# Kernel optimization log

Measured on AMD Instinct MI355X. Metric: run time of the kernel, lower is better.

## Reference

```python
import jax, jax.numpy as jnp
import numpy as np

N = 50000   # num_nodes
E = 640000  # num_edges (avg degree ~12.8)
D = 128     # input_dim
H = 128     # hidden_dim
T = 100     # targets per head


def setup_inputs() -> dict:
    key = jax.random.key(0)
    ks = jax.random.split(key, 20)
    w = lambda k, s: jax.random.normal(k, s, jnp.float32) * 0.02
    return {
        "x": jax.random.normal(ks[0], (N, D), jnp.float32),
        "edge_index": jax.random.randint(ks[1], (2, E), 0, N, dtype=jnp.int32),
        "edge_weight": jax.random.uniform(ks[2], (E,), jnp.float32),
        "ace_idx": jax.random.randint(ks[3], (T,), 0, N, dtype=jnp.int32),
        "h2_idx": jax.random.randint(ks[4], (T,), 0, N, dtype=jnp.int32),
        "W1": w(ks[5], (D, H)), "b1": jnp.zeros((H,), jnp.float32),
        "W2": w(ks[6], (H, H)), "b2": jnp.zeros((H,), jnp.float32),
        "W3": w(ks[7], (H, H)), "b3": jnp.zeros((H,), jnp.float32),
        "Wh": w(ks[8], (H, H)), "bh": jnp.zeros((H,), jnp.float32),
        "Wace": w(ks[9], (H, 1)), "bace": jnp.zeros((1,), jnp.float32),
        "Wh2": w(ks[10], (H, 1)), "bh2": jnp.zeros((1,), jnp.float32),
    }


def gcn_conv(x, src, dst, ew, W, b):
    # PyG GCNConv: add self-loops (weight 1), symmetric D^-1/2 (A+I) D^-1/2, then XW + b
    n = x.shape[0]
    xw = x @ W                                             # [N, H]
    deg = jax.ops.segment_sum(ew, dst, num_segments=n) + 1.0  # +1 from self-loop
    dinv = jax.lax.rsqrt(jnp.maximum(deg, 1e-12))          # deg >= 1 here
    norm = dinv[src] * ew * dinv[dst]                      # per-edge coefficient
    agg = jax.ops.segment_sum(norm[:, None] * xw[src], dst, num_segments=n)
    agg = agg + (dinv * dinv)[:, None] * xw                # self-loop contribution
    return agg + b


def reference(x, edge_index, edge_weight, ace_idx, h2_idx,
              W1, b1, W2, b2, W3, b3, Wh, bh, Wace, bace, Wh2, bh2):
    src, dst = edge_index[0], edge_index[1]
    h = jax.nn.relu(gcn_conv(x, src, dst, edge_weight, W1, b1))
    h = jax.nn.relu(gcn_conv(h, src, dst, edge_weight, W2, b2))
    h = jax.nn.relu(gcn_conv(h, src, dst, edge_weight, W3, b3))
    # dropout is identity in eval mode
    h = jax.nn.relu(h @ Wh + bh)
    ace_pred = h[ace_idx] @ Wace + bace   # [T, 1]
    h2_pred = h[h2_idx] @ Wh2 + bh2       # [T, 1]
    return jnp.concatenate([ace_pred, h2_pred], axis=0)  # [2T, 1]
```

## Files before the change

kernel.cpp:

```cpp
#include <hip/hip_runtime.h>
#include <math.h>

constexpr int N = 50000;
constexpr int E = 640000;
constexpr int D = 128;
constexpr int T = 100;
constexpr int NB = (N + 255) / 256;
constexpr int MAXDEG = 64;
constexpr float SC = 256.0f;
constexpr float SCINV = 1.0f / 256.0f;

typedef __attribute__((ext_vector_type(8))) _Float16 half8v;
typedef __attribute__((ext_vector_type(8))) unsigned short ushort8v;
typedef __attribute__((ext_vector_type(4))) float f32x4;


__global__ void edge_pass_kernel(const float* __restrict__ ew, const int* __restrict__ src,
                                 const int* __restrict__ dst,
                                 unsigned long long* __restrict__ degcnt,
                                 unsigned int* __restrict__ slot) {
  int e = blockIdx.x * 256 + threadIdx.x;
  if (e < E) {
    float w = ew[e];
    int d = dst[e];
    unsigned int fxdeg = __float2uint_rn(w * 16777216.0f);
    unsigned int fx16 = __float2uint_rn(w * 65536.0f);
    if (fx16 > 65535u) fx16 = 65535u;
    unsigned long long old = atomicAdd(&degcnt[d],
                                       ((unsigned long long)fxdeg << 32) | 1ull);
    unsigned int rank = (unsigned int)(old & 0xffffffffull);
    if (rank < MAXDEG)
      slot[(size_t)d * MAXDEG + rank] = (fx16 << 16) | (unsigned int)src[e];
  }
}


__global__ __launch_bounds__(256) void prep_kernel(
    const uint2* __restrict__ degcnt, float* __restrict__ dinv,
    const float* __restrict__ W0, const float* __restrict__ W1,
    const float* __restrict__ W2, unsigned short* __restrict__ wt,
    unsigned short* __restrict__ w3kn) {
  if (blockIdx.x < NB) {
    int i = blockIdx.x * 256 + threadIdx.x;
    if (i < N) {
      uint2 p = degcnt[i];
      float d = (float)p.y * (1.0f / 16777216.0f) + 1.0f;
      dinv[i] = 1.0f / sqrtf(d);
    }
  } else {
    int idx = (blockIdx.x - NB) * 256 + threadIdx.x;
    int layer = idx >> 14;
    int r = idx & 16383;
    int k = r & 127, n = r >> 7;
    const float* W = layer == 0 ? W0 : layer == 1 ? W1 : W2;
    float v = W[k * D + n] * (layer == 0 ? SC : 1.0f);
    _Float16 h = (_Float16)v;
    unsigned short bits = *(unsigned short*)&h;
    wt[layer * 16384 + n * D + k] = bits;
    if (layer == 2) w3kn[k * D + n] = bits;
  }
}


__device__ inline void stage_B(const unsigned short* __restrict__ Wt,
                               unsigned short* __restrict__ Bl, int tid) {
  constexpr int SB = 136;
#pragma unroll
  for (int it = 0; it < 8; ++it) {
    int idx = tid + it * 256;
    int r = idx >> 4;
    int c8 = idx & 15;
    ushort8v v = *(const ushort8v*)&Wt[r * D + c8 * 8];
    *(ushort8v*)&Bl[r * SB + c8 * 8] = v;
  }
}

__device__ inline void mfma_core_and_store(
    const unsigned short* __restrict__ Bl, half8v (*a)[2], const float* __restrict__ dinv,
    int row0, int rbase, int q, int n16, unsigned short* __restrict__ out) {
  constexpr int SB = 136;
  f32x4 acc[2][8] = {};
#pragma unroll
  for (int kc = 0; kc < 4; ++kc) {
    const int ko = kc * 32 + q * 8;
#pragma unroll
    for (int ct = 0; ct < 8; ++ct) {
      int n = ct * 16 + n16;
      half8v b = *(const half8v*)&Bl[n * SB + ko];
#pragma unroll
      for (int rt = 0; rt < 2; ++rt) {
        acc[rt][ct] = __builtin_amdgcn_mfma_f32_16x16x32_f16(a[kc][rt], b, acc[rt][ct], 0, 0, 0);
      }
    }
  }
#pragma unroll
  for (int rt = 0; rt < 2; ++rt) {
#pragma unroll
    for (int r = 0; r < 4; ++r) {
      int gr = row0 + rbase + rt * 16 + q * 4 + r;
      if (gr < N) {
        float dv = dinv[gr];
#pragma unroll
        for (int ct = 0; ct < 8; ++ct) {
          int col = ct * 16 + n16;
          _Float16 h = (_Float16)(acc[rt][ct][r] * dv);
          out[(size_t)gr * D + col] = *(unsigned short*)&h;
        }
      }
    }
  }
}

__global__ __launch_bounds__(256) void gemm_mfma_kernel(
    const unsigned short* __restrict__ A, const unsigned short* __restrict__ Wt,
    const float* __restrict__ dinv, unsigned short* __restrict__ out) {
  constexpr int SB = 136;
  __shared__ unsigned short Bl[128 * SB];
  const int tid = threadIdx.x;
  const int row0 = blockIdx.x * 128;
  stage_B(Wt, Bl, tid);
  __syncthreads();

  const int w = tid >> 6, lane = tid & 63;
  const int q = lane >> 4, n16 = lane & 15;
  const int rbase = w * 32;
  size_t arow[2];
#pragma unroll
  for (int rt = 0; rt < 2; ++rt) {
    int gr = row0 + rbase + rt * 16 + n16;
    if (gr >= N) gr = N - 1;
    arow[rt] = (size_t)gr * D;
  }
  half8v a[4][2];
#pragma unroll
  for (int kc = 0; kc < 4; ++kc) {
    const int ko = kc * 32 + q * 8;
#pragma unroll
    for (int rt = 0; rt < 2; ++rt)
      a[kc][rt] = *(const half8v*)&A[arow[rt] + ko];
  }
  mfma_core_and_store(Bl, a, dinv, row0, rbase, q, n16, out);
}

__global__ __launch_bounds__(256) void gemm_mfma_f32_kernel(
    const float* __restrict__ A, const unsigned short* __restrict__ Wt,
    const float* __restrict__ dinv, unsigned short* __restrict__ out) {
  constexpr int SB = 136;
  __shared__ unsigned short Bl[128 * SB];
  const int tid = threadIdx.x;
  const int row0 = blockIdx.x * 128;
  stage_B(Wt, Bl, tid);
  __syncthreads();

  const int w = tid >> 6, lane = tid & 63;
  const int q = lane >> 4, n16 = lane & 15;
  const int rbase = w * 32;
  size_t arow[2];
#pragma unroll
  for (int rt = 0; rt < 2; ++rt) {
    int gr = row0 + rbase + rt * 16 + n16;
    if (gr >= N) gr = N - 1;
    arow[rt] = (size_t)gr * D;
  }
  half8v a[4][2];
#pragma unroll
  for (int kc = 0; kc < 4; ++kc) {
    const int ko = kc * 32 + q * 8;
#pragma unroll
    for (int rt = 0; rt < 2; ++rt) {
      float4 v0 = *(const float4*)&A[arow[rt] + ko];
      float4 v1 = *(const float4*)&A[arow[rt] + ko + 4];
      half8v h;
      h[0] = (_Float16)v0.x; h[1] = (_Float16)v0.y;
      h[2] = (_Float16)v0.z; h[3] = (_Float16)v0.w;
      h[4] = (_Float16)v1.x; h[5] = (_Float16)v1.y;
      h[6] = (_Float16)v1.z; h[7] = (_Float16)v1.w;
      a[kc][rt] = h;
    }
  }
  mfma_core_and_store(Bl, a, dinv, row0, rbase, q, n16, out);
}


__global__ __launch_bounds__(256) void agg_kernel(
    const unsigned short* __restrict__ z, const unsigned int* __restrict__ slot,
    const uint2* __restrict__ degcnt, const float* __restrict__ dinv,
    const float* __restrict__ bias, unsigned short* __restrict__ oP) {
  int g = (blockIdx.x * 256 + threadIdx.x) >> 4;
  int lane = threadIdx.x & 15;

  int cnt = (int)degcnt[g].x; if (cnt > MAXDEG) cnt = MAXDEG;
  half8v xv = *(const half8v*)&z[(size_t)g * D + lane * 8];
  float acc[8];
#pragma unroll
  for (int i = 0; i < 8; ++i) acc[i] = (float)xv[i];

  const unsigned int* sl = slot + (size_t)g * MAXDEG;
  int k = 0;
  for (; k + 2 <= cnt; k += 2) {
    unsigned int p0 = sl[k], p1 = sl[k + 1];
    float c0 = (float)(p0 >> 16) * (1.0f / 65536.0f);
    float c1 = (float)(p1 >> 16) * (1.0f / 65536.0f);
    half8v v0 = *(const half8v*)&z[(size_t)(p0 & 0xffffu) * D + lane * 8];
    half8v v1 = *(const half8v*)&z[(size_t)(p1 & 0xffffu) * D + lane * 8];
#pragma unroll
    for (int i = 0; i < 8; ++i) {
      acc[i] = fmaf(c0, (float)v0[i], acc[i]);
      acc[i] = fmaf(c1, (float)v1[i], acc[i]);
    }
  }
  if (k < cnt) {
    unsigned int p = sl[k];
    float c = (float)(p >> 16) * (1.0f / 65536.0f);
    half8v v = *(const half8v*)&z[(size_t)(p & 0xffffu) * D + lane * 8];
#pragma unroll
    for (int i = 0; i < 8; ++i) acc[i] = fmaf(c, (float)v[i], acc[i]);
  }

  float dv = dinv[g];
  half8v hv;
#pragma unroll
  for (int i = 0; i < 8; ++i)
    hv[i] = (_Float16)fmaxf(fmaf(dv, acc[i], bias[lane * 8 + i] * SC), 0.f);
  *(half8v*)&oP[(size_t)g * D + lane * 8] = hv;
}


__global__ __launch_bounds__(256) void l23_heads_kernel(
    const unsigned short* __restrict__ z2, const unsigned int* __restrict__ slot,
    const uint2* __restrict__ degcnt, const float* __restrict__ dinv,
    const float* __restrict__ b2, const float* __restrict__ b3,
    const unsigned short* __restrict__ w3kn,
    const float* __restrict__ Wh, const float* __restrict__ bh,
    const int* __restrict__ ace_idx, const int* __restrict__ h2_idx,
    const float* __restrict__ Wace, const float* __restrict__ bace,
    const float* __restrict__ Wh2, const float* __restrict__ bh2,
    float* __restrict__ out) {
  __shared__ float sacc[16][128];
  __shared__ unsigned short w3l[16384];
  __shared__ float svec[128];
  __shared__ float h3v[128];
  __shared__ float psum[2];
  int t = blockIdx.x;
  int tid = threadIdx.x;
  int node; const float* whead; float bhead;
  if (t < T) { node = ace_idx[t];     whead = Wace; bhead = bace[0]; }
  else       { node = h2_idx[t - T];  whead = Wh2;  bhead = bh2[0]; }

#pragma unroll
  for (int it = 0; it < 8; ++it) {
    int idx = tid + it * 256;
    *(ushort8v*)&w3l[idx * 8] = *(const ushort8v*)&w3kn[idx * 8];
  }

  int grp = tid >> 4, lane = tid & 15;
  float b2l[8];
#pragma unroll
  for (int i = 0; i < 8; ++i) b2l[i] = b2[lane * 8 + i] * SC;

  int tcnt = (int)degcnt[node].x; if (tcnt > MAXDEG) tcnt = MAXDEG;
  const unsigned int* tsl = slot + (size_t)node * MAXDEG;
  int nitems = 1 + tcnt;
  float a[8] = {};
  for (int it = grp; it < nitems; it += 16) {
    int u; float wgt;
    if (it == 0) { u = node; wgt = 1.0f; }
    else {
      unsigned int p = tsl[it - 1];
      wgt = (float)(p >> 16) * (1.0f / 65536.0f);
      u = (int)(p & 0xffffu);
    }
    float dvu = dinv[u];
    half8v xv = *(const half8v*)&z2[(size_t)u * D + lane * 8];
    float r[8];
#pragma unroll
    for (int i = 0; i < 8; ++i) r[i] = (float)xv[i];
    int cu = (int)degcnt[u].x; if (cu > MAXDEG) cu = MAXDEG;
    const unsigned int* usl = slot + (size_t)u * MAXDEG;
    for (int e = 0; e < cu; ++e) {
      unsigned int p2 = usl[e];
      float c2 = (float)(p2 >> 16) * (1.0f / 65536.0f);
      half8v v = *(const half8v*)&z2[(size_t)(p2 & 0xffffu) * D + lane * 8];
#pragma unroll
      for (int i = 0; i < 8; ++i) r[i] = fmaf(c2, (float)v[i], r[i]);
    }
#pragma unroll
    for (int i = 0; i < 8; ++i) {
      float h2 = fmaxf(fmaf(dvu, r[i], b2l[i]), 0.f);
      a[i] = fmaf(wgt, dvu * h2, a[i]);
    }
  }
#pragma unroll
  for (int i = 0; i < 8; ++i) sacc[grp][lane * 8 + i] = a[i];
  __syncthreads();

  if (tid < 128) {
    float s = 0.f;
#pragma unroll
    for (int gp = 0; gp < 16; ++gp) s += sacc[gp][tid];
    svec[tid] = s * dinv[node];
  }
  __syncthreads();

  if (tid < 128) {
    float y = b3[tid] * SC;
#pragma unroll 16
    for (int k = 0; k < 128; ++k) {
      _Float16 wv = *(const _Float16*)&w3l[k * D + tid];
      y = fmaf(svec[k], (float)wv, y);
    }
    h3v[tid] = fmaxf(y, 0.f) * SCINV;
  }
  __syncthreads();

  float v = 0.f;
  if (tid < 128) {
    float acc = bh[tid];
#pragma unroll 16
    for (int k = 0; k < 128; ++k)
      acc = fmaf(h3v[k], Wh[k * D + tid], acc);
    v = fmaxf(acc, 0.f) * whead[tid];
  }
#pragma unroll
  for (int off = 32; off; off >>= 1) v += __shfl_down(v, off, 64);
  if (tid < 128 && (tid & 63) == 0) psum[tid >> 6] = v;
  __syncthreads();
  if (tid == 0) out[t] = psum[0] + psum[1] + bhead;
}


extern "C" void kernel_launch(void* const* d_in, const int* in_sizes, int n_in,
                              void* d_out, int out_size, void* d_ws, size_t ws_size,
                              hipStream_t stream) {
  const float* x    = (const float*)d_in[0];
  const int*   ei   = (const int*)d_in[1];
  const float* ew   = (const float*)d_in[2];
  const int*   ace  = (const int*)d_in[3];
  const int*   h2   = (const int*)d_in[4];
  const float* W1 = (const float*)d_in[5];  const float* b1 = (const float*)d_in[6];
  const float* W2 = (const float*)d_in[7];  const float* b2 = (const float*)d_in[8];
  const float* W3 = (const float*)d_in[9];  const float* b3 = (const float*)d_in[10];
  const float* Wh = (const float*)d_in[11]; const float* bh = (const float*)d_in[12];
  const float* Wace = (const float*)d_in[13]; const float* bace = (const float*)d_in[14];
  const float* Wh2  = (const float*)d_in[15]; const float* bh2  = (const float*)d_in[16];
  const int* src = ei;
  const int* dst = ei + E;

  char* w = (char*)d_ws;
  unsigned long long* degcnt = (unsigned long long*)w;  w += (size_t)N * 8;
  float* dinv   = (float*)w;              w += N * 4;
  unsigned int* slot = (unsigned int*)w;  w += (size_t)N * MAXDEG * 4;
  unsigned short* wt = (unsigned short*)w; w += 3 * 16384 * 2;
  unsigned short* w3kn = (unsigned short*)w; w += 16384 * 2;
  unsigned short* zbuf = (unsigned short*)w; w += (size_t)N * D * 2;
  unsigned short* P1  = (unsigned short*)w; w += (size_t)N * D * 2;

  hipMemsetAsync(degcnt, 0, (size_t)N * 8, stream);
  edge_pass_kernel<<<(E + 255) / 256, 256, 0, stream>>>(ew, src, dst, degcnt, slot);
  prep_kernel<<<NB + 192, 256, 0, stream>>>((const uint2*)degcnt, dinv, W1, W2, W3, wt, w3kn);

  const int GB = (N + 127) / 128;
  const int AG = N * 16 / 256;

  gemm_mfma_f32_kernel<<<GB, 256, 0, stream>>>(x, wt + 0 * 16384, dinv, zbuf);
  agg_kernel<<<AG, 256, 0, stream>>>(zbuf, slot, (const uint2*)degcnt, dinv, b1, P1);
  gemm_mfma_kernel<<<GB, 256, 0, stream>>>(P1, wt + 1 * 16384, dinv, zbuf);
  l23_heads_kernel<<<2 * T, 256, 0, stream>>>(zbuf, slot, (const uint2*)degcnt, dinv,
                                              b2, b3, w3kn, Wh, bh, ace, h2,
                                              Wace, bace, Wh2, bh2, (float*)d_out);
}
```

Measured before the change: 224.0 us.

## Fuse layer-1 aggregation into layer-2 GEMM via LDS tile

Merges the aggregation kernel and the second MFMA GEMM into one kernel. Each block aggregates 128 rows into an LDS tile, then runs the GEMM from LDS. This drops the intermediate P1 write and read through global memory, plus one launch. In exchange each block uses about 70KB of LDS, which lowers occupancy. The gather phase also runs in 8 serial passes per block, with fewer gather threads in flight than the standalone aggregation kernel had.

```diff
diff --git a/kernel.cpp b/kernel.cpp
--- a/kernel.cpp
+++ b/kernel.cpp
@@ -111,36 +111,6 @@
   }
 }
 
-__global__ __launch_bounds__(256) void gemm_mfma_kernel(
-    const unsigned short* __restrict__ A, const unsigned short* __restrict__ Wt,
-    const float* __restrict__ dinv, unsigned short* __restrict__ out) {
-  constexpr int SB = 136;
-  __shared__ unsigned short Bl[128 * SB];
-  const int tid = threadIdx.x;
-  const int row0 = blockIdx.x * 128;
-  stage_B(Wt, Bl, tid);
-  __syncthreads();
-
-  const int w = tid >> 6, lane = tid & 63;
-  const int q = lane >> 4, n16 = lane & 15;
-  const int rbase = w * 32;
-  size_t arow[2];
-#pragma unroll
-  for (int rt = 0; rt < 2; ++rt) {
-    int gr = row0 + rbase + rt * 16 + n16;
-    if (gr >= N) gr = N - 1;
-    arow[rt] = (size_t)gr * D;
-  }
-  half8v a[4][2];
-#pragma unroll
-  for (int kc = 0; kc < 4; ++kc) {
-    const int ko = kc * 32 + q * 8;
-#pragma unroll
-    for (int rt = 0; rt < 2; ++rt)
-      a[kc][rt] = *(const half8v*)&A[arow[rt] + ko];
-  }
-  mfma_core_and_store(Bl, a, dinv, row0, rbase, q, n16, out);
-}
 
 __global__ __launch_bounds__(256) void gemm_mfma_f32_kernel(
     const float* __restrict__ A, const unsigned short* __restrict__ Wt,
@@ -182,47 +152,76 @@
 }
 
 
-__global__ __launch_bounds__(256) void agg_kernel(
-    const unsigned short* __restrict__ z, const unsigned int* __restrict__ slot,
+__global__ __launch_bounds__(256) void agg_gemm_kernel(
+    const unsigned short* __restrict__ z1, const unsigned int* __restrict__ slot,
     const uint2* __restrict__ degcnt, const float* __restrict__ dinv,
-    const float* __restrict__ bias, unsigned short* __restrict__ oP) {
-  int g = (blockIdx.x * 256 + threadIdx.x) >> 4;
-  int lane = threadIdx.x & 15;
-
-  int cnt = (int)degcnt[g].x; if (cnt > MAXDEG) cnt = MAXDEG;
-  half8v xv = *(const half8v*)&z[(size_t)g * D + lane * 8];
-  float acc[8];
-#pragma unroll
-  for (int i = 0; i < 8; ++i) acc[i] = (float)xv[i];
-
-  const unsigned int* sl = slot + (size_t)g * MAXDEG;
-  int k = 0;
-  for (; k + 2 <= cnt; k += 2) {
-    unsigned int p0 = sl[k], p1 = sl[k + 1];
-    float c0 = (float)(p0 >> 16) * (1.0f / 65536.0f);
-    float c1 = (float)(p1 >> 16) * (1.0f / 65536.0f);
-    half8v v0 = *(const half8v*)&z[(size_t)(p0 & 0xffffu) * D + lane * 8];
-    half8v v1 = *(const half8v*)&z[(size_t)(p1 & 0xffffu) * D + lane * 8];
+    const float* __restrict__ bias, const unsigned short* __restrict__ Wt,
+    unsigned short* __restrict__ out) {
+  constexpr int SB = 136;
+  __shared__ unsigned short Bl[128 * SB];
+  __shared__ unsigned short Xl[128 * SB];
+  const int tid = threadIdx.x;
+  const int row0 = blockIdx.x * 128;
+  stage_B(Wt, Bl, tid);
+
+  const int grp = tid >> 4, lane = tid & 15;
+  float bl[8];
+#pragma unroll
+  for (int i = 0; i < 8; ++i) bl[i] = bias[lane * 8 + i] * SC;
+
+#pragma unroll
+  for (int pass = 0; pass < 8; ++pass) {
+    int r = pass * 16 + grp;
+    int g = row0 + r; if (g >= N) g = N - 1;
+    int cnt = (int)degcnt[g].x; if (cnt > MAXDEG) cnt = MAXDEG;
+    half8v xv = *(const half8v*)&z1[(size_t)g * D + lane * 8];
+    float acc[8];
+#pragma unroll
+    for (int i = 0; i < 8; ++i) acc[i] = (float)xv[i];
+    const unsigned int* sl = slot + (size_t)g * MAXDEG;
+    int k = 0;
+    for (; k + 2 <= cnt; k += 2) {
+      unsigned int p0 = sl[k], p1 = sl[k + 1];
+      float c0 = (float)(p0 >> 16) * (1.0f / 65536.0f);
+      float c1 = (float)(p1 >> 16) * (1.0f / 65536.0f);
+      half8v v0 = *(const half8v*)&z1[(size_t)(p0 & 0xffffu) * D + lane * 8];
+      half8v v1 = *(const half8v*)&z1[(size_t)(p1 & 0xffffu) * D + lane * 8];
+#pragma unroll
+      for (int i = 0; i < 8; ++i) {
+        acc[i] = fmaf(c0, (float)v0[i], acc[i]);
+        acc[i] = fmaf(c1, (float)v1[i], acc[i]);
+      }
+    }
+    if (k < cnt) {
+      unsigned int p = sl[k];
+      float c = (float)(p >> 16) * (1.0f / 65536.0f);
+      half8v v = *(const half8v*)&z1[(size_t)(p & 0xffffu) * D + lane * 8];
+#pragma unroll
+      for (int i = 0; i < 8; ++i) acc[i] = fmaf(c, (float)v[i], acc[i]);
+    }
+    float dv = dinv[g];
+    ushort8v hv;
 #pragma unroll
     for (int i = 0; i < 8; ++i) {
-      acc[i] = fmaf(c0, (float)v0[i], acc[i]);
-      acc[i] = fmaf(c1, (float)v1[i], acc[i]);
-    }
-  }
-  if (k < cnt) {
-    unsigned int p = sl[k];
-    float c = (float)(p >> 16) * (1.0f / 65536.0f);
-    half8v v = *(const half8v*)&z[(size_t)(p & 0xffffu) * D + lane * 8];
-#pragma unroll
-    for (int i = 0; i < 8; ++i) acc[i] = fmaf(c, (float)v[i], acc[i]);
-  }
-
-  float dv = dinv[g];
-  half8v hv;
-#pragma unroll
-  for (int i = 0; i < 8; ++i)
-    hv[i] = (_Float16)fmaxf(fmaf(dv, acc[i], bias[lane * 8 + i] * SC), 0.f);
-  *(half8v*)&oP[(size_t)g * D + lane * 8] = hv;
+      _Float16 h = (_Float16)fmaxf(fmaf(dv, acc[i], bl[i]), 0.f);
+      hv[i] = *(unsigned short*)&h;
+    }
+    *(ushort8v*)&Xl[r * SB + lane * 8] = hv;
+  }
+  __syncthreads();
+
+  const int w = tid >> 6, lane64 = tid & 63;
+  const int q = lane64 >> 4, n16 = lane64 & 15;
+  const int rbase = w * 32;
+  half8v a[4][2];
+#pragma unroll
+  for (int kc = 0; kc < 4; ++kc) {
+    const int ko = kc * 32 + q * 8;
+#pragma unroll
+    for (int rt = 0; rt < 2; ++rt)
+      a[kc][rt] = *(const half8v*)&Xl[(rbase + rt * 16 + n16) * SB + ko];
+  }
+  mfma_core_and_store(Bl, a, dinv, row0, rbase, q, n16, out);
 }
 
 
@@ -352,20 +351,19 @@
   unsigned int* slot = (unsigned int*)w;  w += (size_t)N * MAXDEG * 4;
   unsigned short* wt = (unsigned short*)w; w += 3 * 16384 * 2;
   unsigned short* w3kn = (unsigned short*)w; w += 16384 * 2;
-  unsigned short* zbuf = (unsigned short*)w; w += (size_t)N * D * 2;
-  unsigned short* P1  = (unsigned short*)w; w += (size_t)N * D * 2;
+  unsigned short* z1 = (unsigned short*)w; w += (size_t)N * D * 2;
+  unsigned short* z2 = (unsigned short*)w; w += (size_t)N * D * 2;
 
   hipMemsetAsync(degcnt, 0, (size_t)N * 8, stream);
   edge_pass_kernel<<<(E + 255) / 256, 256, 0, stream>>>(ew, src, dst, degcnt, slot);
   prep_kernel<<<NB + 192, 256, 0, stream>>>((const uint2*)degcnt, dinv, W1, W2, W3, wt, w3kn);
 
   const int GB = (N + 127) / 128;
-  const int AG = N * 16 / 256;
-
-  gemm_mfma_f32_kernel<<<GB, 256, 0, stream>>>(x, wt + 0 * 16384, dinv, zbuf);
-  agg_kernel<<<AG, 256, 0, stream>>>(zbuf, slot, (const uint2*)degcnt, dinv, b1, P1);
-  gemm_mfma_kernel<<<GB, 256, 0, stream>>>(P1, wt + 1 * 16384, dinv, zbuf);
-  l23_heads_kernel<<<2 * T, 256, 0, stream>>>(zbuf, slot, (const uint2*)degcnt, dinv,
+
+  gemm_mfma_f32_kernel<<<GB, 256, 0, stream>>>(x, wt + 0 * 16384, dinv, z1);
+  agg_gemm_kernel<<<GB, 256, 0, stream>>>(z1, slot, (const uint2*)degcnt, dinv,
+                                          b1, wt + 1 * 16384, z2);
+  l23_heads_kernel<<<2 * T, 256, 0, stream>>>(z2, slot, (const uint2*)degcnt, dinv,
                                               b2, b3, w3kn, Wh, bh, ace, h2,
                                               Wace, bace, Wh2, bh2, (float*)d_out);
 }
```

Measured after the change: 245.6 us. +9.7%, slower.
